# Optimization experiments

Measured on AMD Instinct MI355X. Metric: run time of the kernel, lower is better.

## Reference

```python
import jax, jax.numpy as jnp
import numpy as np
import math

B, N, D_MODEL = 1, 2925, 1536
NUM_HEADS, HEAD_DIM = 12, 128
F, H, W = 13, 15, 15
MAX_SEQ = 1024
EPS = 1e-6


def _make_freqs(max_seq, dim):
    # (cos, sin) pairs for half-dim rotary frequencies, base 10000
    inv = 1.0 / (10000.0 ** (np.arange(0, dim, 2, dtype=np.float64) / dim))
    ang = np.arange(max_seq, dtype=np.float64)[:, None] * inv[None, :]
    return jnp.asarray(np.stack([np.cos(ang), np.sin(ang)], axis=-1), dtype=jnp.float32)


def setup_inputs() -> dict:
    key = jax.random.key(0)
    ks = jax.random.split(key, 10)
    s = 1.0 / math.sqrt(D_MODEL)
    dim_base = HEAD_DIM // 6              # 21
    dim_t = HEAD_DIM - 4 * dim_base       # 44
    dim_h = 2 * dim_base                  # 42
    return {
        "x": jax.random.normal(ks[0], (B, N, D_MODEL), dtype=jnp.float32),
        "Wq": jax.random.normal(ks[1], (D_MODEL, D_MODEL), dtype=jnp.float32) * s,
        "bq": jnp.zeros((D_MODEL,), dtype=jnp.float32),
        "Wk": jax.random.normal(ks[2], (D_MODEL, D_MODEL), dtype=jnp.float32) * s,
        "bk": jnp.zeros((D_MODEL,), dtype=jnp.float32),
        "Wv": jax.random.normal(ks[3], (D_MODEL, D_MODEL), dtype=jnp.float32) * s,
        "bv": jnp.zeros((D_MODEL,), dtype=jnp.float32),
        "Wo": jax.random.normal(ks[4], (D_MODEL, D_MODEL), dtype=jnp.float32) * s,
        "bo": jnp.zeros((D_MODEL,), dtype=jnp.float32),
        "q_scale": jnp.ones((D_MODEL,), dtype=jnp.float32),
        "k_scale": jnp.ones((D_MODEL,), dtype=jnp.float32),
        "freqs_t": _make_freqs(MAX_SEQ, dim_t),
        "freqs_h": _make_freqs(MAX_SEQ, dim_h),
        "freqs_w": _make_freqs(MAX_SEQ, dim_h),
        "f": F, "h": H, "w": W,
    }


def _rms_norm(x, scale, eps=EPS):
    var = jnp.mean(jnp.square(x), axis=-1, keepdims=True)
    return x * jax.lax.rsqrt(var + eps) * scale


def _rope_apply(x, f, h, w, freqs_t, freqs_h, freqs_w):
    # x: [b, n, H, D] with n == f*h*w
    b, n, nh, d = x.shape
    db = d // 6
    dt, dh, dw = d - 4 * db, 2 * db, 2 * db
    ft = jnp.broadcast_to(freqs_t[:f, None, None, :, :], (f, h, w, dt // 2, 2))
    fh = jnp.broadcast_to(freqs_h[None, :h, None, :, :], (f, h, w, dh // 2, 2))
    fw = jnp.broadcast_to(freqs_w[None, None, :w, :, :], (f, h, w, dw // 2, 2))
    fg = jnp.concatenate([ft, fh, fw], axis=3).reshape(n, d // 2, 2)[None, :, None, :, :]
    xc = x.reshape(b, n, nh, d // 2, 2)
    re = xc[..., 0] * fg[..., 0] - xc[..., 1] * fg[..., 1]
    im = xc[..., 0] * fg[..., 1] + xc[..., 1] * fg[..., 0]
    return jnp.stack([re, im], axis=-1).reshape(b, n, nh, d)


def reference(x, Wq, bq, Wk, bk, Wv, bv, Wo, bo, q_scale, k_scale,
              freqs_t, freqs_h, freqs_w, f, h, w):
    b, n, _ = x.shape
    nh, d = NUM_HEADS, HEAD_DIM
    # projections + RMSNorm across full hidden dim (before head split)
    q = _rms_norm(x @ Wq + bq, q_scale).reshape(b, n, nh, d)
    k = _rms_norm(x @ Wk + bk, k_scale).reshape(b, n, nh, d)
    v = (x @ Wv + bv).reshape(b, n, nh, d)
    # 3D RoPE on [b, n, H, D] layout
    q = _rope_apply(q, f, h, w, freqs_t, freqs_h, freqs_w)
    k = _rope_apply(k, f, h, w, freqs_t, freqs_h, freqs_w)
    # [b, H, n, d]
    q = q.transpose(0, 2, 1, 3)
    k = k.transpose(0, 2, 1, 3)
    v = v.transpose(0, 2, 1, 3)
    scores = jnp.einsum("bhid,bhjd->bhij", q, k) / math.sqrt(d)
    attn = jax.nn.softmax(scores, axis=-1)
    out = jnp.einsum("bhij,bhjd->bhid", attn, v)
    out = out.transpose(0, 2, 1, 3).reshape(b, n, nh * d)
    return out @ Wo + bo
```

## Files before the change

kernel.cpp:

```cpp
#include <hip/hip_runtime.h>


#define N_TOK 2925
#define DMODEL 1536
#define NHEAD 12
#define HDIM 128
#define KSPLIT 1472
#define VT_STRIDE 2944

typedef __attribute__((ext_vector_type(8))) __bf16 bf16x8;
typedef __attribute__((ext_vector_type(4))) float floatx4;

#define MFMA(a, b, c) __builtin_amdgcn_mfma_f32_16x16x32_bf16((a), (b), (c), 0, 0, 0)

static __device__ __forceinline__ unsigned short f2bf(float f) {
    unsigned u = __builtin_bit_cast(unsigned, f);
    return (unsigned short)((u + 0x7fffu + ((u >> 16) & 1u)) >> 16);
}

static __device__ __forceinline__ void gload_lds16(const unsigned short* g, unsigned short* l) {
    __builtin_amdgcn_global_load_lds((const __attribute__((address_space(1))) void*)g,
                                     (__attribute__((address_space(3))) void*)l, 16, 0, 0);
}

__global__ __launch_bounds__(256) void k_convert_x(const float* __restrict__ x,
                                                   unsigned short* __restrict__ xb, int n) {
    int i = (blockIdx.x * 256 + threadIdx.x) * 4;
    if (i < n) {
        float4 v = *(const float4*)(x + i);
        uint2 o;
        o.x = (unsigned)f2bf(v.x) | ((unsigned)f2bf(v.y) << 16);
        o.y = (unsigned)f2bf(v.z) | ((unsigned)f2bf(v.w) << 16);
        *(uint2*)(xb + i) = o;
    }
}

__global__ __launch_bounds__(256) void k_transpose_w(const float* __restrict__ W0,
                                                     const float* __restrict__ W1,
                                                     const float* __restrict__ W2,
                                                     const float* __restrict__ W3,
                                                     unsigned short* __restrict__ Wt) {
    __shared__ float tile[32][33];
    const float* W = blockIdx.z == 0 ? W0 : blockIdx.z == 1 ? W1 : blockIdx.z == 2 ? W2 : W3;
    unsigned short* out = Wt + (size_t)blockIdx.z * DMODEL * DMODEL;
    int tx = threadIdx.x, ty = threadIdx.y;
    int bx = blockIdx.x * 32, by = blockIdx.y * 32;
#pragma unroll
    for (int i = 0; i < 4; i++)
        tile[ty + 8 * i][tx] = W[(size_t)(by + ty + 8 * i) * DMODEL + bx + tx];
    __syncthreads();
#pragma unroll
    for (int i = 0; i < 4; i++)
        out[(size_t)(bx + ty + 8 * i) * DMODEL + by + tx] = f2bf(tile[tx][ty + 8 * i]);
}

__global__ __launch_bounds__(256, 2) void k_gemm(const unsigned short* __restrict__ A,
                                                 const unsigned short* __restrict__ BtBase,
                                                 const float* __restrict__ b0,
                                                 const float* __restrict__ b1,
                                                 const float* __restrict__ b2,
                                                 float* __restrict__ Cbase, int M) {
    const int z = blockIdx.z;
    const unsigned short* Bt = BtBase + (size_t)z * DMODEL * DMODEL;
    const float* bias = (z == 0) ? b0 : (z == 1) ? b1 : b2;
    float* C = Cbase + (size_t)z * M * DMODEL;

    __shared__ __align__(16) unsigned short As[128 * 32];
    __shared__ __align__(16) unsigned short Bs[128 * 32];

    const int tid = threadIdx.x;
    const int wave = tid >> 6, lane = tid & 63, quad = lane >> 4, l16 = lane & 15;
    const int wr = wave >> 1, wc = wave & 1;
    const int m0 = blockIdx.y * 128, n0 = blockIdx.x * 128;

    const int r4 = tid >> 2, c4 = (tid & 3) * 8;

    floatx4 acc[4][4] = {};

    for (int k0 = 0; k0 < DMODEL; k0 += 32) {
        gload_lds16(A + (size_t)(m0 + r4) * DMODEL + k0 + c4,       &As[r4 * 32 + c4]);
        gload_lds16(A + (size_t)(m0 + r4 + 64) * DMODEL + k0 + c4,  &As[(r4 + 64) * 32 + c4]);
        gload_lds16(Bt + (size_t)(n0 + r4) * DMODEL + k0 + c4,      &Bs[r4 * 32 + c4]);
        gload_lds16(Bt + (size_t)(n0 + r4 + 64) * DMODEL + k0 + c4, &Bs[(r4 + 64) * 32 + c4]);
        __syncthreads();

        bf16x8 af[4], bfm[4];
#pragma unroll
        for (int i = 0; i < 4; i++)
            af[i] = *(const bf16x8*)&As[(wr * 64 + i * 16 + l16) * 32 + quad * 8];
#pragma unroll
        for (int j = 0; j < 4; j++)
            bfm[j] = *(const bf16x8*)&Bs[(wc * 64 + j * 16 + l16) * 32 + quad * 8];
#pragma unroll
        for (int i = 0; i < 4; i++)
#pragma unroll
            for (int j = 0; j < 4; j++)
                acc[i][j] = MFMA(af[i], bfm[j], acc[i][j]);
        __syncthreads();
    }

#pragma unroll
    for (int j = 0; j < 4; j++) {
        int cg = n0 + wc * 64 + j * 16 + l16;
        float bv = bias[cg];
#pragma unroll
        for (int i = 0; i < 4; i++) {
            int rbase = m0 + wr * 64 + i * 16 + quad * 4;
#pragma unroll
            for (int r = 0; r < 4; r++) {
                int rg = rbase + r;
                if (rg < M) C[(size_t)rg * DMODEL + cg] = acc[i][j][r] + bv;
            }
        }
    }
}

__global__ __launch_bounds__(256) void k_norm_rope(const float* __restrict__ Qf,
                                                   const float* __restrict__ Kf,
                                                   const float* __restrict__ Vf,
                                                   const float* __restrict__ qsc,
                                                   const float* __restrict__ ksc,
                                                   const float* __restrict__ ft,
                                                   const float* __restrict__ fh,
                                                   const float* __restrict__ fw,
                                                   unsigned short* __restrict__ qb,
                                                   unsigned short* __restrict__ kb,
                                                   unsigned short* __restrict__ vb) {
    const int n = blockIdx.x;
    const int tid = threadIdx.x, wave = tid >> 6, lane = tid & 63;
    const int t_i = n / 225, rem = n % 225, h_i = rem / 15, w_i = rem % 15;
    const float att_scale = 0.08838834764831845f * 1.4426950408889634f;

    float2 qv[3], kv[3], vv[3];
    float sq = 0.f, sk = 0.f;
#pragma unroll
    for (int c = 0; c < 3; c++) {
        int p = tid + 256 * c;
        qv[c] = *(const float2*)(Qf + (size_t)n * DMODEL + 2 * p);
        kv[c] = *(const float2*)(Kf + (size_t)n * DMODEL + 2 * p);
        vv[c] = *(const float2*)(Vf + (size_t)n * DMODEL + 2 * p);
        sq += qv[c].x * qv[c].x + qv[c].y * qv[c].y;
        sk += kv[c].x * kv[c].x + kv[c].y * kv[c].y;
    }
#pragma unroll
    for (int off = 32; off >= 1; off >>= 1) {
        sq += __shfl_xor(sq, off, 64);
        sk += __shfl_xor(sk, off, 64);
    }
    __shared__ float red[2][4];
    if (lane == 0) { red[0][wave] = sq; red[1][wave] = sk; }
    __syncthreads();
    sq = red[0][0] + red[0][1] + red[0][2] + red[0][3];
    sk = red[1][0] + red[1][1] + red[1][2] + red[1][3];
    const float rq = rsqrtf(sq * (1.f / 1536.f) + 1e-6f) * att_scale;
    const float rk = rsqrtf(sk * (1.f / 1536.f) + 1e-6f);

#pragma unroll
    for (int c = 0; c < 3; c++) {
        int p = tid + 256 * c;
        int hd = p >> 6, pl = p & 63, dd = 2 * pl;
        float cs, sn;
        if (pl < 22)      { cs = ft[t_i * 44 + 2 * pl];        sn = ft[t_i * 44 + 2 * pl + 1]; }
        else if (pl < 43) { int pp = pl - 22; cs = fh[h_i * 42 + 2 * pp]; sn = fh[h_i * 42 + 2 * pp + 1]; }
        else              { int pp = pl - 43; cs = fw[w_i * 42 + 2 * pp]; sn = fw[w_i * 42 + 2 * pp + 1]; }
        int hidx = hd * 128 + dd;
        float q0 = qv[c].x * rq * qsc[hidx], q1 = qv[c].y * rq * qsc[hidx + 1];
        float k0 = kv[c].x * rk * ksc[hidx], k1 = kv[c].y * rk * ksc[hidx + 1];
        size_t o = ((size_t)hd * N_TOK + n) * HDIM + dd;
        unsigned qo = (unsigned)f2bf(q0 * cs - q1 * sn) | ((unsigned)f2bf(q0 * sn + q1 * cs) << 16);
        unsigned ko = (unsigned)f2bf(k0 * cs - k1 * sn) | ((unsigned)f2bf(k0 * sn + k1 * cs) << 16);
        unsigned vo = (unsigned)f2bf(vv[c].x) | ((unsigned)f2bf(vv[c].y) << 16);
        *(unsigned*)(qb + o) = qo;
        *(unsigned*)(kb + o) = ko;
        *(unsigned*)(vb + o) = vo;
    }
}

__global__ __launch_bounds__(256) void k_transpose_v(const unsigned short* __restrict__ vbi,
                                                     unsigned short* __restrict__ vt) {
    __shared__ unsigned short tile[32][33];
    const int head = blockIdx.z;
    const int t0 = blockIdx.x * 32, d0 = blockIdx.y * 32;
    const int tx = threadIdx.x, ty = threadIdx.y;
#pragma unroll
    for (int i = 0; i < 4; i++) {
        int t = t0 + ty + 8 * i;
        tile[ty + 8 * i][tx] = (t < N_TOK) ? vbi[((size_t)head * N_TOK + t) * HDIM + d0 + tx] : 0;
    }
    __syncthreads();
    int t = t0 + tx;
#pragma unroll
    for (int i = 0; i < 4; i++)
        vt[((size_t)head * HDIM + d0 + ty + 8 * i) * VT_STRIDE + t] = tile[tx][ty + 8 * i];
}

__global__ __launch_bounds__(256, 3) void k_attn_part(const unsigned short* __restrict__ qb,
                                                      const unsigned short* __restrict__ kb,
                                                      const unsigned short* __restrict__ vt,
                                                      float* __restrict__ Opart,
                                                      float* __restrict__ mbuf,
                                                      float* __restrict__ lbuf) {
    __shared__ unsigned short Ks[64 * 136];
    __shared__ unsigned short Vs[128 * 72];
    __shared__ unsigned short Ps[4][16 * 72];

    const int tid = threadIdx.x, wave = tid >> 6, lane = tid & 63;
    const int quad = lane >> 4, l16 = lane & 15;
    const int head = blockIdx.y, z = blockIdx.z;
    const int q0 = blockIdx.x * 64 + wave * 16;
    const unsigned short* qh = qb + (size_t)head * N_TOK * HDIM;
    const unsigned short* kh = kb + (size_t)head * N_TOK * HDIM;
    const unsigned short* vh = vt + (size_t)head * HDIM * VT_STRIDE;
    unsigned short* ps = Ps[wave];

    const int kbeg = z ? KSPLIT : 0;
    const int kend = z ? N_TOK : KSPLIT;

    bf16x8 aq[4];
    {
        int qrow = q0 + l16;
        if (qrow < N_TOK) {
#pragma unroll
            for (int ks = 0; ks < 4; ks++)
                aq[ks] = *(const bf16x8*)&qh[(size_t)qrow * HDIM + ks * 32 + quad * 8];
        } else {
#pragma unroll
            for (int ks = 0; ks < 4; ks++) aq[ks] = (bf16x8)(__bf16)0.0f;
        }
    }

    floatx4 oacc[8] = {};
    float m_r[4] = {-1e30f, -1e30f, -1e30f, -1e30f};
    float l_r[4] = {0.f, 0.f, 0.f, 0.f};

    for (int kb0 = kbeg; kb0 < kend; kb0 += 64) {
#pragma unroll
        for (int c = 0; c < 4; c++) {
            int chunk = tid + 256 * c;
            int row = chunk >> 4, col = (chunk & 15) * 8;
            int gk = kb0 + row; if (gk >= N_TOK) gk = N_TOK - 1;
            *(uint4*)&Ks[row * 136 + col] = *(const uint4*)(kh + (size_t)gk * HDIM + col);
        }
#pragma unroll
        for (int c = 0; c < 4; c++) {
            int chunk = tid + 256 * c;
            int d = chunk >> 3, col = (chunk & 7) * 8;
            *(uint4*)&Vs[d * 72 + col] = *(const uint4*)(vh + (size_t)d * VT_STRIDE + kb0 + col);
        }
        __syncthreads();

        floatx4 sa[4] = {};
#pragma unroll
        for (int j = 0; j < 4; j++) {
            bf16x8 bkf[4];
#pragma unroll
            for (int ks = 0; ks < 4; ks++)
                bkf[ks] = *(const bf16x8*)&Ks[(j * 16 + l16) * 136 + ks * 32 + quad * 8];
#pragma unroll
            for (int ks = 0; ks < 4; ks++)
                sa[j] = MFMA(aq[ks], bkf[ks], sa[j]);
        }

        bool valid[4];
#pragma unroll
        for (int j = 0; j < 4; j++) valid[j] = (kb0 + j * 16 + l16) < kend;

        float alpha[4];
#pragma unroll
        for (int r = 0; r < 4; r++) {
            float x = -1e30f;
#pragma unroll
            for (int j = 0; j < 4; j++) x = fmaxf(x, valid[j] ? sa[j][r] : -1e30f);
#pragma unroll
            for (int off = 8; off >= 1; off >>= 1) x = fmaxf(x, __shfl_xor(x, off, 16));
            float mnew = fmaxf(m_r[r], x);
            alpha[r] = exp2f(m_r[r] - mnew);
            m_r[r] = mnew;
        }
        float rsum[4] = {0.f, 0.f, 0.f, 0.f};
#pragma unroll
        for (int j = 0; j < 4; j++)
#pragma unroll
            for (int r = 0; r < 4; r++) {
                float p = valid[j] ? exp2f(sa[j][r] - m_r[r]) : 0.f;
                rsum[r] += p;
                ps[(quad * 4 + r) * 72 + j * 16 + l16] = f2bf(p);
            }
#pragma unroll
        for (int r = 0; r < 4; r++) {
            float s = rsum[r];
#pragma unroll
            for (int off = 8; off >= 1; off >>= 1) s += __shfl_xor(s, off, 16);
            l_r[r] = l_r[r] * alpha[r] + s;
        }
#pragma unroll
        for (int jd = 0; jd < 8; jd++)
#pragma unroll
            for (int r = 0; r < 4; r++) oacc[jd][r] *= alpha[r];

#pragma unroll
        for (int ks = 0; ks < 2; ks++) {
            bf16x8 ap = *(const bf16x8*)&ps[l16 * 72 + ks * 32 + quad * 8];
#pragma unroll
            for (int jd = 0; jd < 8; jd++) {
                bf16x8 bvf = *(const bf16x8*)&Vs[(jd * 16 + l16) * 72 + ks * 32 + quad * 8];
                oacc[jd] = MFMA(ap, bvf, oacc[jd]);
            }
        }
        __syncthreads();
    }

#pragma unroll
    for (int r = 0; r < 4; r++) {
        int rg = q0 + quad * 4 + r;
        if (rg < N_TOK) {
            size_t rbase = ((size_t)(z * NHEAD + head) * N_TOK + rg) * HDIM;
#pragma unroll
            for (int jd = 0; jd < 8; jd++)
                Opart[rbase + jd * 16 + l16] = oacc[jd][r];
            if (l16 == 0) {
                int mi = (z * NHEAD + head) * N_TOK + rg;
                mbuf[mi] = m_r[r];
                lbuf[mi] = l_r[r];
            }
        }
    }
}

__global__ __launch_bounds__(256) void k_combine(const float* __restrict__ Opart,
                                                 const float* __restrict__ mbuf,
                                                 const float* __restrict__ lbuf,
                                                 unsigned short* __restrict__ ab) {
    const int R = NHEAD * N_TOK;
    int r = blockIdx.x * 8 + (threadIdx.x >> 5);
    if (r >= R) return;
    int l32 = threadIdx.x & 31;
    float m0 = mbuf[r], m1 = mbuf[R + r];
    float l0 = lbuf[r], l1 = lbuf[R + r];
    float m = fmaxf(m0, m1);
    float w0 = exp2f(m0 - m), w1 = exp2f(m1 - m);
    float inv = 1.f / (l0 * w0 + l1 * w1);
    w0 *= inv; w1 *= inv;
    float4 a = *(const float4*)&Opart[(size_t)r * HDIM + l32 * 4];
    float4 b = *(const float4*)&Opart[((size_t)R + r) * HDIM + l32 * 4];
    int head = r / N_TOK, tok = r % N_TOK;
    unsigned short* o = ab + (size_t)tok * DMODEL + head * HDIM + l32 * 4;
    uint2 pk;
    pk.x = (unsigned)f2bf(a.x * w0 + b.x * w1) | ((unsigned)f2bf(a.y * w0 + b.y * w1) << 16);
    pk.y = (unsigned)f2bf(a.z * w0 + b.z * w1) | ((unsigned)f2bf(a.w * w0 + b.w * w1) << 16);
    *(uint2*)o = pk;
}

extern "C" void kernel_launch(void* const* d_in, const int* in_sizes, int n_in,
                              void* d_out, int out_size, void* d_ws, size_t ws_size,
                              hipStream_t stream) {
    const float* x   = (const float*)d_in[0];
    const float* Wq  = (const float*)d_in[1];
    const float* bq  = (const float*)d_in[2];
    const float* Wk  = (const float*)d_in[3];
    const float* bk  = (const float*)d_in[4];
    const float* Wv  = (const float*)d_in[5];
    const float* bv  = (const float*)d_in[6];
    const float* Wo  = (const float*)d_in[7];
    const float* bo  = (const float*)d_in[8];
    const float* qsc = (const float*)d_in[9];
    const float* ksc = (const float*)d_in[10];
    const float* ft  = (const float*)d_in[11];
    const float* fh  = (const float*)d_in[12];
    const float* fw  = (const float*)d_in[13];

    char* ws = (char*)d_ws;
    unsigned short* xb   = (unsigned short*)ws; ws += (size_t)N_TOK * DMODEL * 2;
    unsigned short* Wt   = (unsigned short*)ws; ws += (size_t)4 * DMODEL * DMODEL * 2;
    unsigned short* ab   = (unsigned short*)ws; ws += (size_t)N_TOK * DMODEL * 2;
    char* qkvf_region    = ws;                  ws += (size_t)3 * N_TOK * DMODEL * 4;
    unsigned short* qkvb = (unsigned short*)ws; ws += (size_t)3 * N_TOK * DMODEL * 2;

    float* Qf = (float*)qkvf_region;
    float* Kf = Qf + (size_t)N_TOK * DMODEL;
    float* Vf = Qf + (size_t)2 * N_TOK * DMODEL;
    float* Opart = (float*)qkvf_region;
    float* mbuf  = Opart + (size_t)2 * NHEAD * N_TOK * HDIM;
    float* lbuf  = mbuf + (size_t)2 * NHEAD * N_TOK;
    unsigned short* vtp = (unsigned short*)(lbuf + (size_t)2 * NHEAD * N_TOK);

    unsigned short* qbp = qkvb;
    unsigned short* kbp = qkvb + (size_t)N_TOK * DMODEL;
    unsigned short* vbp = qkvb + (size_t)2 * N_TOK * DMODEL;

    const int nelem = N_TOK * DMODEL;
    k_convert_x<<<(nelem / 4 + 255) / 256, 256, 0, stream>>>(x, xb, nelem);
    k_transpose_w<<<dim3(48, 48, 4), dim3(32, 8), 0, stream>>>(Wq, Wk, Wv, Wo, Wt);
    k_gemm<<<dim3(12, 23, 3), 256, 0, stream>>>(xb, Wt, bq, bk, bv, Qf, N_TOK);
    k_norm_rope<<<N_TOK, 256, 0, stream>>>(Qf, Kf, Vf, qsc, ksc, ft, fh, fw, qbp, kbp, vbp);
    k_transpose_v<<<dim3(92, 4, NHEAD), dim3(32, 8), 0, stream>>>(vbp, vtp);
    k_attn_part<<<dim3(46, NHEAD, 2), 256, 0, stream>>>(qbp, kbp, vtp, Opart, mbuf, lbuf);
    k_combine<<<(NHEAD * N_TOK + 7) / 8, 256, 0, stream>>>(Opart, mbuf, lbuf, ab);
    k_gemm<<<dim3(12, 23, 1), 256, 0, stream>>>(ab, Wt + (size_t)3 * DMODEL * DMODEL,
                                                bo, bo, bo, (float*)d_out, N_TOK);
}
```

Before: 421.8 us.

## Use direct global-to-LDS loads with XOR-swizzled tiles and lazy softmax rescaling

```diff
diff --git a/kernel.cpp b/kernel.cpp
--- a/kernel.cpp
+++ b/kernel.cpp
@@ -194,18 +194,18 @@
         vt[((size_t)head * HDIM + d0 + ty + 8 * i) * VT_STRIDE + t] = tile[tx][ty + 8 * i];
 }
 
-__global__ __launch_bounds__(256, 3) void k_attn_part(const unsigned short* __restrict__ qb,
+__global__ __launch_bounds__(256, 4) void k_attn_part(const unsigned short* __restrict__ qb,
                                                       const unsigned short* __restrict__ kb,
                                                       const unsigned short* __restrict__ vt,
                                                       float* __restrict__ Opart,
                                                       float* __restrict__ mbuf,
                                                       float* __restrict__ lbuf) {
-    __shared__ unsigned short Ks[64 * 136];
-    __shared__ unsigned short Vs[128 * 72];
-    __shared__ unsigned short Ps[4][16 * 72];
+    __shared__ __align__(16) unsigned short Ks[64 * 128];
+    __shared__ __align__(16) unsigned short Vs[128 * 64];
+    __shared__ __align__(16) unsigned short Ps[4][16 * 64];
 
     const int tid = threadIdx.x, wave = tid >> 6, lane = tid & 63;
-    const int quad = lane >> 4, l16 = lane & 15;
+    const int quad = lane >> 4, l16 = lane & 15, x7 = l16 & 7;
     const int head = blockIdx.y, z = blockIdx.z;
     const int q0 = blockIdx.x * 64 + wave * 16;
     const unsigned short* qh = qb + (size_t)head * N_TOK * HDIM;
@@ -216,6 +216,20 @@
     const int kbeg = z ? KSPLIT : 0;
     const int kend = z ? N_TOK : KSPLIT;
 
+    int koff[4];
+#pragma unroll
+    for (int ks = 0; ks < 4; ks++) {
+        int c = ks * 4 + quad;
+        koff[ks] = ((c & 8) | ((c & 7) ^ x7)) * 8;
+    }
+
+    const int krow = tid >> 4, ksw = tid & 15;
+    const int kc = (ksw & 8) | ((ksw & 7) ^ (krow & 7));
+    const int vd = tid >> 3, vsw = tid & 7;
+    const int vc = vsw ^ (vd & 7);
+    const unsigned short* ksrc = kh + (size_t)krow * HDIM + kc * 8;
+    const unsigned short* vsrc = vh + (size_t)vd * VT_STRIDE + vc * 8;
+
     bf16x8 aq[4];
     {
         int qrow = q0 + l16;
@@ -234,81 +248,116 @@
     float l_r[4] = {0.f, 0.f, 0.f, 0.f};
 
     for (int kb0 = kbeg; kb0 < kend; kb0 += 64) {
-#pragma unroll
-        for (int c = 0; c < 4; c++) {
-            int chunk = tid + 256 * c;
-            int row = chunk >> 4, col = (chunk & 15) * 8;
-            int gk = kb0 + row; if (gk >= N_TOK) gk = N_TOK - 1;
-            *(uint4*)&Ks[row * 136 + col] = *(const uint4*)(kh + (size_t)gk * HDIM + col);
-        }
-#pragma unroll
-        for (int c = 0; c < 4; c++) {
-            int chunk = tid + 256 * c;
-            int d = chunk >> 3, col = (chunk & 7) * 8;
-            *(uint4*)&Vs[d * 72 + col] = *(const uint4*)(vh + (size_t)d * VT_STRIDE + kb0 + col);
-        }
+        const bool fullt = (kb0 + 64 <= kend);
+
+        if (fullt) {
+#pragma unroll
+            for (int i = 0; i < 4; i++)
+                gload_lds16(ksrc + (size_t)(kb0 + 16 * i) * HDIM, &Ks[(tid + 256 * i) * 8]);
+        } else {
+#pragma unroll
+            for (int i = 0; i < 4; i++) {
+                int gk = kb0 + krow + 16 * i;
+                gk = gk < N_TOK ? gk : N_TOK - 1;
+                gload_lds16(kh + (size_t)gk * HDIM + kc * 8, &Ks[(tid + 256 * i) * 8]);
+            }
+        }
+#pragma unroll
+        for (int i = 0; i < 4; i++)
+            gload_lds16(vsrc + (size_t)(32 * i) * VT_STRIDE + kb0, &Vs[(tid + 256 * i) * 8]);
         __syncthreads();
 
         floatx4 sa[4] = {};
 #pragma unroll
-        for (int j = 0; j < 4; j++) {
-            bf16x8 bkf[4];
-#pragma unroll
-            for (int ks = 0; ks < 4; ks++)
-                bkf[ks] = *(const bf16x8*)&Ks[(j * 16 + l16) * 136 + ks * 32 + quad * 8];
-#pragma unroll
-            for (int ks = 0; ks < 4; ks++)
-                sa[j] = MFMA(aq[ks], bkf[ks], sa[j]);
-        }
-
+        for (int j = 0; j < 4; j++)
+#pragma unroll
+            for (int ks = 0; ks < 4; ks++) {
+                bf16x8 bkf = *(const bf16x8*)&Ks[(j * 16 + l16) * HDIM + koff[ks]];
+                sa[j] = MFMA(aq[ks], bkf, sa[j]);
+            }
+
+        float xm[4];
         bool valid[4];
-#pragma unroll
-        for (int j = 0; j < 4; j++) valid[j] = (kb0 + j * 16 + l16) < kend;
-
-        float alpha[4];
-#pragma unroll
-        for (int r = 0; r < 4; r++) {
-            float x = -1e30f;
-#pragma unroll
-            for (int j = 0; j < 4; j++) x = fmaxf(x, valid[j] ? sa[j][r] : -1e30f);
-#pragma unroll
-            for (int off = 8; off >= 1; off >>= 1) x = fmaxf(x, __shfl_xor(x, off, 16));
-            float mnew = fmaxf(m_r[r], x);
-            alpha[r] = exp2f(m_r[r] - mnew);
-            m_r[r] = mnew;
-        }
+        if (fullt) {
+#pragma unroll
+            for (int r = 0; r < 4; r++)
+                xm[r] = fmaxf(fmaxf(sa[0][r], sa[1][r]), fmaxf(sa[2][r], sa[3][r]));
+        } else {
+#pragma unroll
+            for (int j = 0; j < 4; j++) valid[j] = (kb0 + j * 16 + l16) < kend;
+#pragma unroll
+            for (int r = 0; r < 4; r++) {
+                float x = -1e30f;
+#pragma unroll
+                for (int j = 0; j < 4; j++) x = fmaxf(x, valid[j] ? sa[j][r] : -1e30f);
+                xm[r] = x;
+            }
+        }
+#pragma unroll
+        for (int r = 0; r < 4; r++)
+#pragma unroll
+            for (int off = 8; off >= 1; off >>= 1)
+                xm[r] = fmaxf(xm[r], __shfl_xor(xm[r], off, 16));
+
+        bool need = false;
+#pragma unroll
+        for (int r = 0; r < 4; r++) need |= (xm[r] > m_r[r] + 8.f);
+        if (__any(need)) {
+#pragma unroll
+            for (int r = 0; r < 4; r++) {
+                float mn = fmaxf(m_r[r], xm[r]);
+                float a = exp2f(m_r[r] - mn);
+                m_r[r] = mn;
+                l_r[r] *= a;
+#pragma unroll
+                for (int jd = 0; jd < 8; jd++) oacc[jd][r] *= a;
+            }
+        }
+
         float rsum[4] = {0.f, 0.f, 0.f, 0.f};
-#pragma unroll
-        for (int j = 0; j < 4; j++)
-#pragma unroll
-            for (int r = 0; r < 4; r++) {
-                float p = valid[j] ? exp2f(sa[j][r] - m_r[r]) : 0.f;
-                rsum[r] += p;
-                ps[(quad * 4 + r) * 72 + j * 16 + l16] = f2bf(p);
-            }
-#pragma unroll
-        for (int r = 0; r < 4; r++) {
-            float s = rsum[r];
-#pragma unroll
-            for (int off = 8; off >= 1; off >>= 1) s += __shfl_xor(s, off, 16);
-            l_r[r] = l_r[r] * alpha[r] + s;
-        }
-#pragma unroll
-        for (int jd = 0; jd < 8; jd++)
-#pragma unroll
-            for (int r = 0; r < 4; r++) oacc[jd][r] *= alpha[r];
+        const int phi = l16 >> 3;
+        const int pq4 = (quad & 1) * 4;
+        if (fullt) {
+#pragma unroll
+            for (int j = 0; j < 4; j++)
+#pragma unroll
+                for (int r = 0; r < 4; r++) {
+                    float p = exp2f(sa[j][r] - m_r[r]);
+                    rsum[r] += p;
+                    ps[(quad * 4 + r) * 64 + (((j * 2 + phi) ^ (pq4 + r)) << 3) + x7] =
+                        __builtin_bit_cast(unsigned short, (__bf16)p);
+                }
+        } else {
+#pragma unroll
+            for (int j = 0; j < 4; j++)
+#pragma unroll
+                for (int r = 0; r < 4; r++) {
+                    float p = valid[j] ? exp2f(sa[j][r] - m_r[r]) : 0.f;
+                    rsum[r] += p;
+                    ps[(quad * 4 + r) * 64 + (((j * 2 + phi) ^ (pq4 + r)) << 3) + x7] =
+                        __builtin_bit_cast(unsigned short, (__bf16)p);
+                }
+        }
+#pragma unroll
+        for (int r = 0; r < 4; r++) l_r[r] += rsum[r];
 
 #pragma unroll
         for (int ks = 0; ks < 2; ks++) {
-            bf16x8 ap = *(const bf16x8*)&ps[l16 * 72 + ks * 32 + quad * 8];
+            bf16x8 ap = *(const bf16x8*)&ps[l16 * 64 + koff[ks]];
 #pragma unroll
             for (int jd = 0; jd < 8; jd++) {
-                bf16x8 bvf = *(const bf16x8*)&Vs[(jd * 16 + l16) * 72 + ks * 32 + quad * 8];
+                bf16x8 bvf = *(const bf16x8*)&Vs[(jd * 16 + l16) * 64 + koff[ks]];
                 oacc[jd] = MFMA(ap, bvf, oacc[jd]);
             }
         }
         __syncthreads();
     }
+
+#pragma unroll
+    for (int r = 0; r < 4; r++)
+#pragma unroll
+        for (int off = 8; off >= 1; off >>= 1)
+            l_r[r] += __shfl_xor(l_r[r], off, 16);
 
 #pragma unroll
     for (int r = 0; r < 4; r++) {
```

Result: faster. 395.0 us (-6.4%).
